# Optimization experiments

Measured on AMD Instinct MI355X. Metric: run time of the kernel, lower is better.

## Reference

```python
import jax, jax.numpy as jnp
import numpy as np
from jax import lax


def _conv1d(z, w):
    # z: [B, C_in, L], w: [C_out, C_in, K], stride 1, padding 1 -> [B, C_out, L]
    return lax.conv_general_dilated(
        z, w, window_strides=(1,), padding=[(1, 1)],
        dimension_numbers=("NCH", "OIH", "NCH"))


def setup_inputs() -> dict:
    key = jax.random.key(0)
    k1, k2, k3 = jax.random.split(key, 3)
    B, T, C, H, L, K = 16, 64, 128, 256, 128, 3
    x = jax.random.normal(k1, (B, T, C, L), dtype=jnp.float32)
    # small init so tanh stays in its useful range
    W_i = jax.random.normal(k2, (H, C, K), dtype=jnp.float32) * 0.05
    W_h = jax.random.normal(k3, (H, H, K), dtype=jnp.float32) * 0.05
    return {"x": x, "W_i": W_i, "W_h": W_h}


def reference(x, W_i, W_h):
    # Conv1DRnn, single layer, unidirectional, no bias, mode RNN_TANH:
    #   h_t = tanh(conv_i(x_t) + conv_h(h_{t-1}))
    # x: [B, T, C, L] -> out: [B, T, H, L]
    B, T, C, L = x.shape
    H = W_i.shape[0]
    h0 = jnp.zeros((B, H, L), dtype=x.dtype)
    xt = jnp.swapaxes(x, 0, 1)  # [T, B, C, L]

    def step(h, x_t):
        h_new = jnp.tanh(_conv1d(x_t, W_i) + _conv1d(h, W_h))
        return h_new, h_new

    _, hs = lax.scan(step, h0, xt)  # hs: [T, B, H, L]
    return jnp.swapaxes(hs, 0, 1)   # [B, T, H, L]
```

## Files before the change

### kernel.cpp

```cpp
#include <hip/hip_runtime.h>
#include <math.h>

typedef _Float16 f16;
typedef _Float16 f16x8 __attribute__((ext_vector_type(8)));
typedef float f32x4 __attribute__((ext_vector_type(4)));
typedef unsigned long long u64;

#define LDIM 128
#define HOUT 256

__device__ __forceinline__ float tanh_fast(float x) {
    float a = fabsf(x);
    float e = __expf(-2.0f * a);
    float r = (1.0f - e) / (1.0f + e);
    return copysignf(r, x);
}

__device__ __forceinline__ void  st_agent(float* p, float v) {
    __hip_atomic_store(p, v, __ATOMIC_RELAXED, __HIP_MEMORY_SCOPE_AGENT);
}
__device__ __forceinline__ float ld_agent(const float* p) {
    return __hip_atomic_load(p, __ATOMIC_RELAXED, __HIP_MEMORY_SCOPE_AGENT);
}
__device__ __forceinline__ u64   ld_agent64(const u64* p) {
    return __hip_atomic_load(p, __ATOMIC_RELAXED, __HIP_MEMORY_SCOPE_AGENT);
}

__global__ void prep_w(const float* __restrict__ wi, f16* __restrict__ wti,
                       const float* __restrict__ wh, f16* __restrict__ wt2h)
{
    int idx = blockIdx.x * 256 + threadIdx.x;
    const int ni = 3 * HOUT * 128;
    if (idx < ni) {
        int k = idx / (HOUT * 128);
        int r = idx - k * (HOUT * 128);
        int h = r >> 7, c = r & 127;
        wti[idx] = (f16)wi[(h * 128 + c) * 3 + k];
    } else {
        int e = idx - ni;
        if (e >= 3 * HOUT * 256) return;
        int j    = e & 7;
        int lane = (e >> 3) & 63;
        int h16  = (e >> 9) & 15;
        int kk   = (e >> 13) & 7;
        int s    = e >> 16;
        int hh = h16 * 16 + (lane & 15);
        int c  = kk * 32 + (lane >> 4) * 8 + j;
        wt2h[e] = (f16)wh[(hh * 256 + c) * 3 + s];
    }
}

__global__ __launch_bounds__(256, 4)
void conv_i_all(const float* __restrict__ x, const f16* __restrict__ wt,
                float* __restrict__ out)
{
    __shared__ __align__(16) char smem[33792];
    const int tid = threadIdx.x;
    const int lane = tid & 63, wid = tid >> 6;
    const int wh = wid >> 1, wl = wid & 1;
    const int n   = blockIdx.x & 1023;
    const int sub = blockIdx.x >> 10;
    const int h0  = (sub >> 1) * 64;
    const int Lb  = (sub & 1) * 64;
    const int l16 = lane & 15, g = lane >> 4;

    const float* actn = x + (long)n * (128 * LDIM);

    {
        const int c4 = tid >> 4;
        const int rb = tid & 15;
        const int lg = Lb + rb * 4;
        f32x4 v[8];
#pragma unroll
        for (int ci = 0; ci < 8; ++ci)
            v[ci] = *(const f32x4*)(actn + (c4 * 8 + ci) * LDIM + lg);
#pragma unroll
        for (int i = 0; i < 4; ++i) {
            int r = rb * 4 + i + 1;
            f16x8 hi, lo;
#pragma unroll
            for (int ci = 0; ci < 8; ++ci) {
                float xx = v[ci][i];
                f16 h = (f16)xx;
                hi[ci] = h;
                lo[ci] = (f16)(xx - (float)h);
            }
            int base = r * 256 + ((c4 ^ (r & 7)) << 4);
            *(f16x8*)(smem + base) = hi;
            *(f16x8*)(smem + 16896 + base) = lo;
        }
        int cl = tid & 127, e = tid >> 7;
        int r = e ? 65 : 0;
        int lg2 = Lb + r - 1;
        float xx = ((unsigned)lg2 < 128u) ? actn[cl * LDIM + lg2] : 0.f;
        f16 h = (f16)xx;
        f16 lo = (f16)(xx - (float)h);
        int off = r * 256 + ((((cl >> 3) ^ (r & 7)) << 4)) + (cl & 7) * 2;
        *(f16*)(smem + off) = h;
        *(f16*)(smem + 16896 + off) = lo;
    }
    __syncthreads();

    f32x4 acc[2][2] = {};
#pragma unroll
    for (int kk = 0; kk < 4; ++kk) {
        f16x8 afr[3][2];
#pragma unroll
        for (int s = 0; s < 3; ++s)
#pragma unroll
            for (int hf = 0; hf < 2; ++hf) {
                int hh = h0 + wh * 32 + hf * 16 + l16;
                afr[s][hf] = *(const f16x8*)(wt + ((s * HOUT + hh) << 7) + kk * 32 + g * 8);
            }
#pragma unroll
        for (int s = 0; s < 3; ++s) {
            f16x8 bfr[2][2];
#pragma unroll
            for (int lf = 0; lf < 2; ++lf) {
                int r = wl * 32 + lf * 16 + l16 + s;
                int base = r * 256 + ((((kk * 4 + g) ^ (r & 7)) << 4));
                bfr[lf][0] = *(const f16x8*)(smem + base);
                bfr[lf][1] = *(const f16x8*)(smem + 16896 + base);
            }
#pragma unroll
            for (int hf = 0; hf < 2; ++hf)
#pragma unroll
                for (int lf = 0; lf < 2; ++lf) {
                    acc[hf][lf] = __builtin_amdgcn_mfma_f32_16x16x32_f16(
                        afr[s][hf], bfr[lf][0], acc[hf][lf], 0, 0, 0);
                    acc[hf][lf] = __builtin_amdgcn_mfma_f32_16x16x32_f16(
                        afr[s][hf], bfr[lf][1], acc[hf][lf], 0, 0, 0);
                }
        }
    }

    float* outn = out + (long)n * (HOUT * LDIM);
#pragma unroll
    for (int hf = 0; hf < 2; ++hf)
#pragma unroll
        for (int lf = 0; lf < 2; ++lf)
#pragma unroll
            for (int vv = 0; vv < 4; ++vv) {
                int hh = h0 + wh * 32 + hf * 16 + g * 4 + vv;
                int ll = Lb + wl * 32 + lf * 16 + l16;
                outn[hh * LDIM + ll] = acc[hf][lf][vv];
            }
}

__global__ __launch_bounds__(256, 1)
void rnn_persist(const f16* __restrict__ wt2, float* __restrict__ out,
                 unsigned int* __restrict__ cnt)
{
    __shared__ __align__(16) char smem[34816];
    const int tid = threadIdx.x;
    const int lane = tid & 63, wid = tid >> 6;
    const int wh = wid >> 1, wl = wid & 1;
    const int b   = blockIdx.x & 15;
    const int sub = blockIdx.x >> 4;
    const int h0  = (sub >> 2) * 64;
    const int Lb  = (sub & 3) * 32;
    const int l16 = lane & 15, g = lane >> 4;
    const long HL = (long)HOUT * LDIM;
    float* outb = out + (long)b * (64 * HL);
    unsigned int* cb = cnt + b * 64;

    f16x8 afr[3][8][2];
#pragma unroll
    for (int s = 0; s < 3; ++s)
#pragma unroll
        for (int kk = 0; kk < 8; ++kk)
#pragma unroll
            for (int hf = 0; hf < 2; ++hf) {
                int h16 = (h0 >> 4) + wh * 2 + hf;
                afr[s][kk][hf] = *(const f16x8*)(wt2 +
                    ((((s * 8 + kk) * 16 + h16) * 64 + lane) << 3));
            }

#pragma unroll
    for (int hf = 0; hf < 2; ++hf)
#pragma unroll
        for (int vv = 0; vv < 4; ++vv) {
            int hh = h0 + wh * 32 + hf * 16 + g * 4 + vv;
            int ll = Lb + wl * 16 + l16;
            long idx = (long)hh * LDIM + ll;
            st_agent(&outb[idx], tanh_fast(outb[idx]));
        }

    for (int t = 1; t < 64; ++t) {
        float* outt = outb + (long)t * HL;
        const float* prev = outb + (long)(t - 1) * HL;

        float zreg[2][4];
#pragma unroll
        for (int hf = 0; hf < 2; ++hf)
#pragma unroll
            for (int vv = 0; vv < 4; ++vv) {
                int hh = h0 + wh * 32 + hf * 16 + g * 4 + vv;
                int ll = Lb + wl * 16 + l16;
                zreg[hf][vv] = outt[(long)hh * LDIM + ll];
            }

        __syncthreads();
        if (tid == 0) {
            __hip_atomic_fetch_add(cb, 1u, __ATOMIC_RELAXED, __HIP_MEMORY_SCOPE_AGENT);
            unsigned int target = 16u * (unsigned)t;
            while (__hip_atomic_load(cb, __ATOMIC_RELAXED,
                                     __HIP_MEMORY_SCOPE_AGENT) < target)
                __builtin_amdgcn_s_sleep(1);
        }
        __syncthreads();
        asm volatile("" ::: "memory");

        {
            const int cq = tid >> 3;
            const int lq = tid & 7;
            const int lg = Lb + lq * 4;
            f32x4 v[8];
#pragma unroll
            for (int ci = 0; ci < 8; ++ci) {
                const u64* p = (const u64*)(prev + (cq * 8 + ci) * LDIM + lg);
                u64 a = ld_agent64(p);
                u64 bq = ld_agent64(p + 1);
                v[ci][0] = __uint_as_float((unsigned)a);
                v[ci][1] = __uint_as_float((unsigned)(a >> 32));
                v[ci][2] = __uint_as_float((unsigned)bq);
                v[ci][3] = __uint_as_float((unsigned)(bq >> 32));
            }
#pragma unroll
            for (int i = 0; i < 4; ++i) {
                int r = lq * 4 + i + 1;
                f16x8 hi, lo;
#pragma unroll
                for (int ci = 0; ci < 8; ++ci) {
                    float xx = v[ci][i];
                    f16 h = (f16)xx;
                    hi[ci] = h;
                    lo[ci] = (f16)(xx - (float)h);
                }
                int base = r * 512 + ((cq ^ (r & 7)) << 4);
                *(f16x8*)(smem + base) = hi;
                *(f16x8*)(smem + 17408 + base) = lo;
            }
            const int cl = tid;
#pragma unroll
            for (int e = 0; e < 2; ++e) {
                int r = e ? 33 : 0;
                int lg2 = Lb + r - 1;
                float xx = ((unsigned)lg2 < 128u) ? ld_agent(&prev[cl * LDIM + lg2]) : 0.f;
                f16 h = (f16)xx;
                f16 lo = (f16)(xx - (float)h);
                int off = r * 512 + ((((cl >> 3) ^ (r & 7)) << 4)) + (cl & 7) * 2;
                *(f16*)(smem + off) = h;
                *(f16*)(smem + 17408 + off) = lo;
            }
        }
        __syncthreads();

        f32x4 acc[2] = {};
#pragma unroll
        for (int kk = 0; kk < 8; ++kk)
#pragma unroll
            for (int s = 0; s < 3; ++s) {
                int r = wl * 16 + l16 + s;
                int base = r * 512 + ((((kk * 4 + g) ^ (r & 7)) << 4));
                f16x8 b0 = *(const f16x8*)(smem + base);
                f16x8 b1 = *(const f16x8*)(smem + 17408 + base);
#pragma unroll
                for (int hf = 0; hf < 2; ++hf) {
                    acc[hf] = __builtin_amdgcn_mfma_f32_16x16x32_f16(
                        afr[s][kk][hf], b0, acc[hf], 0, 0, 0);
                    acc[hf] = __builtin_amdgcn_mfma_f32_16x16x32_f16(
                        afr[s][kk][hf], b1, acc[hf], 0, 0, 0);
                }
            }

#pragma unroll
        for (int hf = 0; hf < 2; ++hf)
#pragma unroll
            for (int vv = 0; vv < 4; ++vv) {
                int hh = h0 + wh * 32 + hf * 16 + g * 4 + vv;
                int ll = Lb + wl * 16 + l16;
                st_agent(&outt[(long)hh * LDIM + ll], tanh_fast(acc[hf][vv] + zreg[hf][vv]));
            }
    }
}

extern "C" void kernel_launch(void* const* d_in, const int* in_sizes, int n_in,
                              void* d_out, int out_size, void* d_ws, size_t ws_size,
                              hipStream_t stream)
{
    const float* x   = (const float*)d_in[0];
    const float* W_i = (const float*)d_in[1];
    const float* W_h = (const float*)d_in[2];
    float* out = (float*)d_out;

    f16* wt_i  = (f16*)d_ws;
    f16* wt2_h = (f16*)((char*)d_ws + 196608);
    unsigned int* cnt = (unsigned int*)((char*)d_ws + 589824);

    prep_w<<<1152, 256, 0, stream>>>(W_i, wt_i, W_h, wt2_h);
    hipMemsetAsync(cnt, 0, 4096, stream);

    conv_i_all<<<8192, 256, 0, stream>>>(x, wt_i, out);
    rnn_persist<<<256, 256, 0, stream>>>(wt2_h, out, cnt);
}
```

Baseline: 433.0 us.

## Replace per-batch counter barrier with neighbor-only flag waits and finer block split

The persistent RNN kernel no longer uses a per-batch atomic counter that every block increments and waits on each timestep. Each block now publishes a per-block step flag, and only waits for the blocks whose previous-step hidden state it reads: all H chunks for its own L tile plus the two neighboring L tiles needed by the width-3 conv. The work split also changes from 256 blocks of 256 threads (32-wide L tiles) to 512 blocks of 128 threads (16-wide L tiles), which halves shared memory per block and adds parallelism. The risk is more, smaller blocks with more redundant halo loads, and a correctness dependence on the flag set being complete and on memory ordering with relaxed atomics.

```diff
diff --git a/kernel.cpp b/kernel.cpp
--- a/kernel.cpp
+++ b/kernel.cpp
@@ -23,6 +23,9 @@
     return __hip_atomic_load(p, __ATOMIC_RELAXED, __HIP_MEMORY_SCOPE_AGENT);
 }
 __device__ __forceinline__ u64   ld_agent64(const u64* p) {
+    return __hip_atomic_load(p, __ATOMIC_RELAXED, __HIP_MEMORY_SCOPE_AGENT);
+}
+__device__ __forceinline__ unsigned ld_flag(const unsigned* p) {
     return __hip_atomic_load(p, __ATOMIC_RELAXED, __HIP_MEMORY_SCOPE_AGENT);
 }
 
@@ -147,22 +150,25 @@
             }
 }
 
-__global__ __launch_bounds__(256, 1)
+__global__ __launch_bounds__(128, 1)
 void rnn_persist(const f16* __restrict__ wt2, float* __restrict__ out,
-                 unsigned int* __restrict__ cnt)
+                 unsigned* __restrict__ flags)
 {
-    __shared__ __align__(16) char smem[34816];
-    const int tid = threadIdx.x;
+    __shared__ __align__(16) char smem[18432];
+    const int tid  = threadIdx.x;
     const int lane = tid & 63, wid = tid >> 6;
-    const int wh = wid >> 1, wl = wid & 1;
-    const int b   = blockIdx.x & 15;
-    const int sub = blockIdx.x >> 4;
-    const int h0  = (sub >> 2) * 64;
-    const int Lb  = (sub & 3) * 32;
-    const int l16 = lane & 15, g = lane >> 4;
-    const long HL = (long)HOUT * LDIM;
+    const int wh   = wid;
+    const int bid  = blockIdx.x;
+    const int b    = bid >> 5;
+    const int sub  = bid & 31;
+    const int h0i  = sub >> 3;
+    const int lbi  = sub & 7;
+    const int h0   = h0i * 64;
+    const int Lb   = lbi * 16;
+    const int l16  = lane & 15, g = lane >> 4;
+    const long HL  = (long)HOUT * LDIM;
     float* outb = out + (long)b * (64 * HL);
-    unsigned int* cb = cnt + b * 64;
+    unsigned* fb = flags + b * 64;
 
     f16x8 afr[3][8][2];
 #pragma unroll
@@ -171,20 +177,31 @@
         for (int kk = 0; kk < 8; ++kk)
 #pragma unroll
             for (int hf = 0; hf < 2; ++hf) {
-                int h16 = (h0 >> 4) + wh * 2 + hf;
+                int h16 = h0i * 4 + wh * 2 + hf;
                 afr[s][kk][hf] = *(const f16x8*)(wt2 +
                     ((((s * 8 + kk) * 16 + h16) * 64 + lane) << 3));
             }
 
+    int dep = sub;
+    if (lane < 12) {
+        int hp = lane & 3;
+        int d  = lane >> 2;
+        int lb2 = lbi + (d == 1 ? -1 : (d == 2 ? 1 : 0));
+        if (lb2 < 0 || lb2 > 7) { hp = h0i; lb2 = lbi; }
+        dep = hp * 8 + lb2;
+    }
+
 #pragma unroll
     for (int hf = 0; hf < 2; ++hf)
 #pragma unroll
         for (int vv = 0; vv < 4; ++vv) {
             int hh = h0 + wh * 32 + hf * 16 + g * 4 + vv;
-            int ll = Lb + wl * 16 + l16;
-            long idx = (long)hh * LDIM + ll;
+            long idx = (long)hh * LDIM + Lb + l16;
             st_agent(&outb[idx], tanh_fast(outb[idx]));
         }
+    __syncthreads();
+    if (tid == 0)
+        __hip_atomic_store(&fb[sub], 1u, __ATOMIC_RELAXED, __HIP_MEMORY_SCOPE_AGENT);
 
     for (int t = 1; t < 64; ++t) {
         float* outt = outb + (long)t * HL;
@@ -196,30 +213,28 @@
 #pragma unroll
             for (int vv = 0; vv < 4; ++vv) {
                 int hh = h0 + wh * 32 + hf * 16 + g * 4 + vv;
-                int ll = Lb + wl * 16 + l16;
-                zreg[hf][vv] = outt[(long)hh * LDIM + ll];
-            }
-
-        __syncthreads();
-        if (tid == 0) {
-            __hip_atomic_fetch_add(cb, 1u, __ATOMIC_RELAXED, __HIP_MEMORY_SCOPE_AGENT);
-            unsigned int target = 16u * (unsigned)t;
-            while (__hip_atomic_load(cb, __ATOMIC_RELAXED,
-                                     __HIP_MEMORY_SCOPE_AGENT) < target)
+                zreg[hf][vv] = outt[(long)hh * LDIM + Lb + l16];
+            }
+
+        if (wid == 0) {
+            unsigned v = (lane < 12) ? ld_flag(&fb[dep]) : 0xFFFFFFFFu;
+            while (__any(v < (unsigned)t)) {
                 __builtin_amdgcn_s_sleep(1);
+                if (lane < 12) v = ld_flag(&fb[dep]);
+            }
         }
         __syncthreads();
         asm volatile("" ::: "memory");
 
         {
-            const int cq = tid >> 3;
-            const int lq = tid & 7;
+            const int cg = tid >> 2;
+            const int lq = tid & 3;
             const int lg = Lb + lq * 4;
             f32x4 v[8];
 #pragma unroll
             for (int ci = 0; ci < 8; ++ci) {
-                const u64* p = (const u64*)(prev + (cq * 8 + ci) * LDIM + lg);
-                u64 a = ld_agent64(p);
+                const u64* p = (const u64*)(prev + (cg * 8 + ci) * LDIM + lg);
+                u64 a  = ld_agent64(p);
                 u64 bq = ld_agent64(p + 1);
                 v[ci][0] = __uint_as_float((unsigned)a);
                 v[ci][1] = __uint_as_float((unsigned)(a >> 32));
@@ -237,21 +252,24 @@
                     hi[ci] = h;
                     lo[ci] = (f16)(xx - (float)h);
                 }
-                int base = r * 512 + ((cq ^ (r & 7)) << 4);
+                int base = r * 512 + ((cg ^ (r & 7)) << 4);
                 *(f16x8*)(smem + base) = hi;
-                *(f16x8*)(smem + 17408 + base) = lo;
-            }
-            const int cl = tid;
+                *(f16x8*)(smem + 9216 + base) = lo;
+            }
 #pragma unroll
             for (int e = 0; e < 2; ++e) {
-                int r = e ? 33 : 0;
-                int lg2 = Lb + r - 1;
-                float xx = ((unsigned)lg2 < 128u) ? ld_agent(&prev[cl * LDIM + lg2]) : 0.f;
-                f16 h = (f16)xx;
-                f16 lo = (f16)(xx - (float)h);
-                int off = r * 512 + ((((cl >> 3) ^ (r & 7)) << 4)) + (cl & 7) * 2;
-                *(f16*)(smem + off) = h;
-                *(f16*)(smem + 17408 + off) = lo;
+                int r = e ? 17 : 0;
+                int lg2 = Lb + (e ? 16 : -1);
+#pragma unroll
+                for (int half = 0; half < 2; ++half) {
+                    int c = tid + half * 128;
+                    float xx = ((unsigned)lg2 < 128u) ? ld_agent(&prev[c * LDIM + lg2]) : 0.f;
+                    f16 h = (f16)xx;
+                    f16 lo = (f16)(xx - (float)h);
+                    int off = r * 512 + ((((c >> 3) ^ (r & 7)) << 4)) + (c & 7) * 2;
+                    *(f16*)(smem + off) = h;
+                    *(f16*)(smem + 9216 + off) = lo;
+                }
             }
         }
         __syncthreads();
@@ -261,10 +279,10 @@
         for (int kk = 0; kk < 8; ++kk)
 #pragma unroll
             for (int s = 0; s < 3; ++s) {
-                int r = wl * 16 + l16 + s;
+                int r = l16 + s;
                 int base = r * 512 + ((((kk * 4 + g) ^ (r & 7)) << 4));
                 f16x8 b0 = *(const f16x8*)(smem + base);
-                f16x8 b1 = *(const f16x8*)(smem + 17408 + base);
+                f16x8 b1 = *(const f16x8*)(smem + 9216 + base);
 #pragma unroll
                 for (int hf = 0; hf < 2; ++hf) {
                     acc[hf] = __builtin_amdgcn_mfma_f32_16x16x32_f16(
@@ -279,9 +297,14 @@
 #pragma unroll
             for (int vv = 0; vv < 4; ++vv) {
                 int hh = h0 + wh * 32 + hf * 16 + g * 4 + vv;
-                int ll = Lb + wl * 16 + l16;
-                st_agent(&outt[(long)hh * LDIM + ll], tanh_fast(acc[hf][vv] + zreg[hf][vv]));
-            }
+                st_agent(&outt[(long)hh * LDIM + Lb + l16],
+                         tanh_fast(acc[hf][vv] + zreg[hf][vv]));
+            }
+
+        __syncthreads();
+        if (tid == 0)
+            __hip_atomic_store(&fb[sub], (unsigned)(t + 1),
+                               __ATOMIC_RELAXED, __HIP_MEMORY_SCOPE_AGENT);
     }
 }
 
@@ -296,11 +319,11 @@
 
     f16* wt_i  = (f16*)d_ws;
     f16* wt2_h = (f16*)((char*)d_ws + 196608);
-    unsigned int* cnt = (unsigned int*)((char*)d_ws + 589824);
+    unsigned* flags = (unsigned*)((char*)d_ws + 589824);
 
     prep_w<<<1152, 256, 0, stream>>>(W_i, wt_i, W_h, wt2_h);
-    hipMemsetAsync(cnt, 0, 4096, stream);
+    hipMemsetAsync(flags, 0, 4096, stream);
 
     conv_i_all<<<8192, 256, 0, stream>>>(x, wt_i, out);
-    rnn_persist<<<256, 256, 0, stream>>>(wt2_h, out, cnt);
-}
+    rnn_persist<<<512, 128, 0, stream>>>(wt2_h, out, flags);
+}
```

Result: slower. 475.2 us (+9.8%).
